# Optimization experiments

Measured on AMD Instinct MI355X. Metric: run time of the kernel, lower is better.

Reference implementation:

```python
import jax, jax.numpy as jnp
import numpy as np

B, S, D, H = 4, 2048, 1024, 16
HD = D // H  # head dim = 64
NEG = jnp.finfo(jnp.float32).min


def setup_inputs() -> dict:
    key = jax.random.key(0)
    ks = jax.random.split(key, 6)
    states = jax.random.normal(ks[0], (B, S, D), dtype=jnp.float32)
    # causal float mask, broadcastable over batch and heads
    mask = jnp.tril(jnp.ones((S, S), dtype=jnp.float32))[None, None, :, :]
    scale = 1.0 / np.sqrt(D)
    Wq = jax.random.normal(ks[1], (D, D), dtype=jnp.float32) * scale
    Wk = jax.random.normal(ks[2], (D, D), dtype=jnp.float32) * scale
    Wv = jax.random.normal(ks[3], (D, D), dtype=jnp.float32) * scale
    Wo = jax.random.normal(ks[4], (D, D), dtype=jnp.float32) * scale
    return {"states": states, "mask": mask, "Wq": Wq, "Wk": Wk, "Wv": Wv, "Wo": Wo}


def _split_heads(x):
    # [B,S,D] -> [B,H,S,HD]
    return x.reshape(B, S, H, HD).transpose(0, 2, 1, 3)


def reference(states, mask, Wq, Wk, Wv, Wo):
    q = _split_heads(states @ Wq)
    k = _split_heads(states @ Wk)
    v = _split_heads(states @ Wv)
    # scores [B,H,S,S], scaled by rsqrt(head_dim) as in the original
    alpha = jnp.einsum("bhqd,bhkd->bhqk", q, k) * (1.0 / jnp.sqrt(jnp.float32(HD)))
    alpha = alpha * mask + (1.0 - mask) * NEG
    alpha = jax.nn.softmax(alpha, axis=-1)
    ctx = jnp.einsum("bhqk,bhkd->bhqd", alpha, v)
    ctx = ctx.transpose(0, 2, 1, 3).reshape(B, S, D)  # concat heads
    return ctx @ Wo
```

## Files before the change

### kernel.cpp

```cpp
#include <hip/hip_runtime.h>
#include <hip/hip_bf16.h>

#define BB 4
#define SS 2048
#define DD 1024
#define HH 16
#define HDD 64
#define MM (BB*SS)

typedef __attribute__((ext_vector_type(8))) short short8;
typedef __attribute__((ext_vector_type(4))) float f32x4;
typedef __attribute__((ext_vector_type(4))) int int4v;
typedef __attribute__((ext_vector_type(4))) short bf16x4;

__device__ __forceinline__ ushort f2bf(float f) {
  union { float f; uint u; } v; v.f = f;
  uint u = v.u;
  uint r = (u + 0x7FFFu + ((u >> 16) & 1u)) >> 16;
  return (ushort)r;
}

__device__ __forceinline__ float exp2f_fast(float x) {
#if __has_builtin(__builtin_amdgcn_exp2f)
  return __builtin_amdgcn_exp2f(x);
#else
  float r; asm("v_exp_f32 %0, %1" : "=v"(r) : "v"(x)); return r;
#endif
}

__device__ __forceinline__ float max3f(float a, float b, float c) {
  return fmaxf(fmaxf(a, b), c);
}

__device__ __forceinline__ bf16x4 pack4bf(float a, float b, float c, float d) {
  union { __hip_bfloat162 h2[2]; bf16x4 s; } u;
  u.h2[0] = __float22bfloat162_rn(make_float2(a, b));
  u.h2[1] = __float22bfloat162_rn(make_float2(c, d));
  return u.s;
}

__device__ __forceinline__ f32x4 mfma16(bf16x4 a, bf16x4 b, f32x4 c) {
#if __has_builtin(__builtin_amdgcn_mfma_f32_16x16x16bf16_1k)
  return __builtin_amdgcn_mfma_f32_16x16x16bf16_1k(a, b, c, 0, 0, 0);
#else
  f32x4 d;
  asm volatile("s_nop 1\n\tv_mfma_f32_16x16x16_bf16 %0, %1, %2, %3\n\ts_nop 7\n\ts_nop 3"
               : "=v"(d) : "v"(a), "v"(b), "v"(c));
  return d;
#endif
}

__device__ __forceinline__ void gload16(void* lds, const void* g) {
  __builtin_amdgcn_global_load_lds((const __attribute__((address_space(1))) void*)g,
                                   (__attribute__((address_space(3))) void*)lds, 16, 0, 0);
}

__global__ __launch_bounds__(256) void k_convert(const float* __restrict__ in,
                                                 ushort* __restrict__ out, int n4) {
  int i = blockIdx.x * 256 + threadIdx.x;
  if (i >= n4) return;
  float4 v = ((const float4*)in)[i];
  uint lo = (uint)f2bf(v.x) | ((uint)f2bf(v.y) << 16);
  uint hi = (uint)f2bf(v.z) | ((uint)f2bf(v.w) << 16);
  ((uint2*)out)[i] = make_uint2(lo, hi);
}

__global__ __launch_bounds__(256) void k_transpose(const float* __restrict__ W0, const float* __restrict__ W1,
                                                   const float* __restrict__ W2, const float* __restrict__ W3,
                                                   ushort* __restrict__ T0, ushort* __restrict__ T1,
                                                   ushort* __restrict__ T2, ushort* __restrict__ T3) {
  __shared__ float t[32][33];
  const float* W; ushort* T;
  switch (blockIdx.z) {
    case 0: W = W0; T = T0; break;
    case 1: W = W1; T = T1; break;
    case 2: W = W2; T = T2; break;
    default: W = W3; T = T3; break;
  }
  float scale = (blockIdx.z == 0) ? 0.18033688011112042f : 1.0f;
  int tx = threadIdx.x, ty = threadIdx.y;
  int x = blockIdx.x * 32 + tx;
  int y0 = blockIdx.y * 32;
#pragma unroll
  for (int j = 0; j < 32; j += 8) t[ty + j][tx] = W[(y0 + ty + j) * DD + x];
  __syncthreads();
#pragma unroll
  for (int j = 0; j < 32; j += 8)
    T[(blockIdx.x * 32 + ty + j) * DD + y0 + tx] = f2bf(t[tx][ty + j] * scale);
}

__global__ __launch_bounds__(256, 2) void k_qkv(const ushort* __restrict__ X,
                                                const ushort* __restrict__ Wqt,
                                                const ushort* __restrict__ Wkt,
                                                const ushort* __restrict__ Wvt,
                                                ushort* __restrict__ Q,
                                                ushort* __restrict__ K,
                                                ushort* __restrict__ Vt) {
  __shared__ ushort Al[2 * 4096];
  __shared__ ushort Bl[3][2 * 4096];
  int tid = threadIdx.x, lane = tid & 63, w = tid >> 6;
  int wm = w >> 1, wn = w & 1, lrow = lane & 15, lgrp = lane >> 4;
  int srow = lane >> 2, scolb = (lane & 3) * 16;
  const char* A8 = (const char*)(X + (size_t)blockIdx.x * 128 * DD);
  const char* B8[3] = { (const char*)(Wqt + (size_t)blockIdx.y * 128 * DD),
                        (const char*)(Wkt + (size_t)blockIdx.y * 128 * DD),
                        (const char*)(Wvt + (size_t)blockIdx.y * 128 * DD) };

  f32x4 acc[3][4][4];
#pragma unroll
  for (int wi = 0; wi < 3; wi++)
#pragma unroll
    for (int i = 0; i < 4; i++)
#pragma unroll
      for (int j = 0; j < 4; j++)
#pragma unroll
        for (int r = 0; r < 4; r++) acc[wi][i][j][r] = 0.f;

#pragma unroll
  for (int ii = 0; ii < 2; ii++) {
    int i = w * 2 + ii;
    size_t ro = (size_t)(i * 16 + srow) * (DD * 2) + scolb;
    gload16(Al + i * 512, A8 + ro);
#pragma unroll
    for (int wi = 0; wi < 3; wi++)
      gload16(&Bl[wi][i * 512], B8[wi] + ro);
  }
  __syncthreads();

  for (int kk = 0; kk < DD; kk += 32) {
    int cur = (kk >> 5) & 1;
    if (kk + 32 < DD) {
#pragma unroll
      for (int ii = 0; ii < 2; ii++) {
        int i = w * 2 + ii;
        size_t ro = (size_t)(i * 16 + srow) * (DD * 2) + (kk + 32) * 2 + scolb;
        gload16(Al + (cur ^ 1) * 4096 + i * 512, A8 + ro);
#pragma unroll
        for (int wi = 0; wi < 3; wi++)
          gload16(&Bl[wi][(cur ^ 1) * 4096 + i * 512], B8[wi] + ro);
      }
    }
    short8 a[4];
#pragma unroll
    for (int i = 0; i < 4; i++)
      a[i] = *(const short8*)&Al[cur * 4096 + (wm * 64 + i * 16 + lrow) * 32 + lgrp * 8];
#pragma unroll
    for (int wi = 0; wi < 3; wi++) {
      short8 b[4];
#pragma unroll
      for (int j = 0; j < 4; j++)
        b[j] = *(const short8*)&Bl[wi][cur * 4096 + (wn * 64 + j * 16 + lrow) * 32 + lgrp * 8];
#pragma unroll
      for (int i = 0; i < 4; i++)
#pragma unroll
        for (int j = 0; j < 4; j++)
          acc[wi][i][j] = __builtin_amdgcn_mfma_f32_16x16x32_bf16(a[i], b[j], acc[wi][i][j], 0, 0, 0);
    }
    __syncthreads();
  }

  int m0 = blockIdx.x * 128 + wm * 64, n0 = blockIdx.y * 128 + wn * 64;
#pragma unroll
  for (int wi = 0; wi < 2; wi++) {
    ushort* Out = (wi == 0) ? Q : K;
#pragma unroll
    for (int i = 0; i < 4; i++)
#pragma unroll
      for (int j = 0; j < 4; j++)
#pragma unroll
        for (int r = 0; r < 4; r++) {
          int row = m0 + i * 16 + lgrp * 4 + r;
          int col = n0 + j * 16 + lrow;
          int b = row >> 11, s = row & 2047, h = col >> 6, hd = col & 63;
          Out[(((size_t)(b * HH + h) * SS) + s) * HDD + hd] = f2bf(acc[wi][i][j][r]);
        }
  }
#pragma unroll
  for (int i = 0; i < 4; i++)
#pragma unroll
    for (int j = 0; j < 4; j++) {
      int row0 = m0 + i * 16 + lgrp * 4;
      int col = n0 + j * 16 + lrow;
      int b = row0 >> 11, s0 = row0 & 2047, h = col >> 6, hd = col & 63;
      bf16x4 s = pack4bf(acc[2][i][j][0], acc[2][i][j][1], acc[2][i][j][2], acc[2][i][j][3]);
      *(bf16x4*)(Vt + (((size_t)(b * HH + h) * HDD) + hd) * SS + s0) = s;
    }
}

#define QB2 64
#define KVB 64
#define NQT2 (SS / QB2)

__global__ __launch_bounds__(128) void k_attn(const ushort* __restrict__ Q,
                                              const ushort* __restrict__ K,
                                              const ushort* __restrict__ Vt,
                                              ushort* __restrict__ Ctx) {
  __shared__ ushort Kl[2][4096];
  __shared__ ushort Vl[2][4096];
  int bid = blockIdx.x;
  int xcd = bid & 7, slot = bid >> 3;
  int j = slot & 15;
  int bh = (slot >> 4) * 8 + xcd;
  int b = bh >> 4, h = bh & 15;
  int tid = threadIdx.x, lane = tid & 63, w = tid >> 6;
  int lrow = lane & 15, lgrp = lane >> 4;

  int srow = lane >> 3;
  int scolb = ((lane & 7) * 16) ^ (srow << 4);
  const char* K8 = (const char*)(K + (size_t)bh * SS * HDD);
  const char* V8 = (const char*)(Vt + (size_t)bh * HDD * SS);

  int kswz = (lrow & 7) << 3;
  int colE[2];
  colE[0] = (lgrp * 8) ^ kswz;
  colE[1] = (lgrp * 8 + 32) ^ kswz;

  const ushort* kc0 = &Kl[0][lrow * 64 + colE[0]];
  const ushort* kc1 = &Kl[0][lrow * 64 + colE[1]];
  const ushort* vbp[4];
#pragma unroll
  for (int t = 0; t < 4; t++) vbp[t] = &Vl[0][lrow * 64 + (((16 * t + lgrp * 4) ^ kswz))];

#pragma unroll
  for (int ph = 0; ph < 2; ph++) {
    int qx = ph == 0 ? (NQT2 - 1 - j) : j;
    int qb = qx * QB2;
    int qw0 = qb + w * 32;
    int ntk = qx + 1;

    const char* kgp[4];
    const char* vgp[4];
#pragma unroll
    for (int ii = 0; ii < 4; ii++) {
      kgp[ii] = K8 + (size_t)(w * 32 + ii * 8 + srow) * 128 + scolb;
      vgp[ii] = V8 + (size_t)(w * 32 + ii * 8 + srow) * (SS * 2) + scolb;
    }

    short8 qf[2][2];
#pragma unroll
    for (int qt = 0; qt < 2; qt++)
#pragma unroll
      for (int c = 0; c < 2; c++)
        qf[qt][c] = *(const short8*)(Q + ((size_t)bh * SS + qb + w * 32 + qt * 16 + lrow) * HDD + lgrp * 8 + 32 * c);

    f32x4 o[2][4];
#pragma unroll
    for (int qt = 0; qt < 2; qt++)
#pragma unroll
      for (int nt = 0; nt < 4; nt++)
#pragma unroll
        for (int r = 0; r < 4; r++) o[qt][nt][r] = 0.f;
    float m_run[2] = {-1e30f, -1e30f}, l_run[2] = {0.f, 0.f};

#pragma unroll
    for (int ii = 0; ii < 4; ii++) {
      gload16(&Kl[0][(w * 4 + ii) * 512], kgp[ii]);
      gload16(&Vl[0][(w * 4 + ii) * 512], vgp[ii]);
      kgp[ii] += KVB * 128;
      vgp[ii] += KVB * 2;
    }
    __syncthreads();

    for (int kt = 0; kt < ntk; kt++) {
      int cur = kt & 1;
      if (kt + 1 < ntk) {
#pragma unroll
        for (int ii = 0; ii < 4; ii++) {
          gload16(&Kl[cur ^ 1][(w * 4 + ii) * 512], kgp[ii]);
          gload16(&Vl[cur ^ 1][(w * 4 + ii) * 512], vgp[ii]);
          kgp[ii] += KVB * 128;
          vgp[ii] += KVB * 2;
        }
      }
      int kb = kt * KVB;
      const ushort* kcc0 = kc0 + (cur << 12);
      const ushort* kcc1 = kc1 + (cur << 12);
      short8 kf[4][2];
#pragma unroll
      for (int t = 0; t < 4; t++) {
        kf[t][0] = *(const short8*)(kcc0 + t * 1024);
        kf[t][1] = *(const short8*)(kcc1 + t * 1024);
      }

      bf16x4 pk[2][4];
#pragma unroll
      for (int qt = 0; qt < 2; qt++) {
        f32x4 st[4];
#pragma unroll
        for (int t = 0; t < 4; t++) {
          f32x4 z;
#pragma unroll
          for (int r = 0; r < 4; r++) z[r] = 0.f;
          z = __builtin_amdgcn_mfma_f32_16x16x32_bf16(kf[t][0], qf[qt][0], z, 0, 0, 0);
          z = __builtin_amdgcn_mfma_f32_16x16x32_bf16(kf[t][1], qf[qt][1], z, 0, 0, 0);
          st[t] = z;
        }
        if (kb + 63 > qw0) {
          int lim = qw0 + qt * 16 + lrow - kb - lgrp * 4;
#pragma unroll
          for (int t = 0; t < 4; t++)
#pragma unroll
            for (int r = 0; r < 4; r++)
              if (16 * t + r > lim) st[t][r] = -1e30f;
        }
        float rm = max3f(st[0][0], st[0][1], st[0][2]);
        rm = max3f(rm, st[0][3], st[1][0]);
        rm = max3f(rm, st[1][1], st[1][2]);
        rm = max3f(rm, st[1][3], st[2][0]);
        rm = max3f(rm, st[2][1], st[2][2]);
        rm = max3f(rm, st[2][3], st[3][0]);
        rm = max3f(rm, st[3][1], st[3][2]);
        rm = fmaxf(rm, st[3][3]);
        rm = fmaxf(rm, __shfl_xor(rm, 16));
        rm = fmaxf(rm, __shfl_xor(rm, 32));
        bool need = rm > m_run[qt] + 8.f;
        if (__any(need)) {
          float mn = need ? rm : m_run[qt];
          float sca = exp2f_fast(m_run[qt] - mn);
          m_run[qt] = mn;
          l_run[qt] *= sca;
#pragma unroll
          for (int nt = 0; nt < 4; nt++)
#pragma unroll
            for (int r = 0; r < 4; r++) o[qt][nt][r] *= sca;
        }
        float m = m_run[qt];
        float rs = 0.f;
#pragma unroll
        for (int t = 0; t < 4; t++) {
          float e0 = exp2f_fast(st[t][0] - m);
          float e1 = exp2f_fast(st[t][1] - m);
          float e2 = exp2f_fast(st[t][2] - m);
          float e3 = exp2f_fast(st[t][3] - m);
          rs += (e0 + e1) + (e2 + e3);
          pk[qt][t] = pack4bf(e0, e1, e2, e3);
        }
        l_run[qt] += rs;
      }

#pragma unroll
      for (int t = 0; t < 4; t++) {
        const ushort* vbt = vbp[t] + (cur << 12);
#pragma unroll
        for (int nt = 0; nt < 4; nt++) {
          bf16x4 va = *(const bf16x4*)(vbt + nt * 1024);
          o[0][nt] = mfma16(va, pk[0][t], o[0][nt]);
          o[1][nt] = mfma16(va, pk[1][t], o[1][nt]);
        }
      }
      __syncthreads();
    }

#pragma unroll
    for (int qt = 0; qt < 2; qt++) {
      float lt = l_run[qt];
      lt += __shfl_xor(lt, 16);
      lt += __shfl_xor(lt, 32);
      float inv = 1.f / lt;
      int q = qb + w * 32 + qt * 16 + lrow;
      ushort* base = Ctx + ((size_t)b * SS + q) * DD + h * HDD;
#pragma unroll
      for (int nt = 0; nt < 4; nt++) {
        bf16x4 s = pack4bf(o[qt][nt][0] * inv, o[qt][nt][1] * inv,
                           o[qt][nt][2] * inv, o[qt][nt][3] * inv);
        *(bf16x4*)(base + nt * 16 + lgrp * 4) = s;
      }
    }
  }
}

__device__ __forceinline__ void gemm_tile(const ushort* __restrict__ Arow,
                                          const ushort* __restrict__ Brow,
                                          ushort* Al, ushort* Bl,
                                          f32x4 acc[4][4]) {
  int tid = threadIdx.x;
  int lane = tid & 63, w = tid >> 6;
  int wm = w >> 1, wn = w & 1;
  int lrow = lane & 15, lgrp = lane >> 4;
#pragma unroll
  for (int i = 0; i < 4; i++)
#pragma unroll
    for (int j = 0; j < 4; j++)
#pragma unroll
      for (int r = 0; r < 4; r++) acc[i][j][r] = 0.f;

  int srow = lane >> 2;
  int scolb = (lane & 3) * 16;
  const char* A8 = (const char*)Arow;
  const char* B8 = (const char*)Brow;

#pragma unroll
  for (int ii = 0; ii < 2; ii++) {
    int i = w * 2 + ii;
    gload16(Al + i * 512, A8 + (size_t)(i * 16 + srow) * (DD * 2) + scolb);
    gload16(Bl + i * 512, B8 + (size_t)(i * 16 + srow) * (DD * 2) + scolb);
  }
  __syncthreads();

  for (int kk = 0; kk < DD; kk += 32) {
    int cur = (kk >> 5) & 1;
    if (kk + 32 < DD) {
#pragma unroll
      for (int ii = 0; ii < 2; ii++) {
        int i = w * 2 + ii;
        gload16(Al + (cur ^ 1) * 4096 + i * 512,
                A8 + (size_t)(i * 16 + srow) * (DD * 2) + (kk + 32) * 2 + scolb);
        gload16(Bl + (cur ^ 1) * 4096 + i * 512,
                B8 + (size_t)(i * 16 + srow) * (DD * 2) + (kk + 32) * 2 + scolb);
      }
    }
    short8 a[4], b[4];
#pragma unroll
    for (int i = 0; i < 4; i++) a[i] = *(const short8*)&Al[cur * 4096 + (wm * 64 + i * 16 + lrow) * 32 + lgrp * 8];
#pragma unroll
    for (int j = 0; j < 4; j++) b[j] = *(const short8*)&Bl[cur * 4096 + (wn * 64 + j * 16 + lrow) * 32 + lgrp * 8];
#pragma unroll
    for (int i = 0; i < 4; i++)
#pragma unroll
      for (int j = 0; j < 4; j++)
        acc[i][j] = __builtin_amdgcn_mfma_f32_16x16x32_bf16(a[i], b[j], acc[i][j], 0, 0, 0);
    __syncthreads();
  }
}

__global__ __launch_bounds__(256) void k_oproj(const ushort* __restrict__ Ctx,
                                               const ushort* __restrict__ Wot,
                                               float* __restrict__ Outp) {
  __shared__ ushort Al[2 * 4096];
  __shared__ ushort Bl[2 * 4096];
  f32x4 acc[4][4];
  gemm_tile(Ctx + (size_t)blockIdx.x * 128 * DD, Wot + (size_t)blockIdx.y * 128 * DD, Al, Bl, acc);
  int lane = threadIdx.x & 63, w = threadIdx.x >> 6;
  int wm = w >> 1, wn = w & 1, lrow = lane & 15, lgrp = lane >> 4;
  int m0 = blockIdx.x * 128 + wm * 64, n0 = blockIdx.y * 128 + wn * 64;
#pragma unroll
  for (int i = 0; i < 4; i++)
#pragma unroll
    for (int j = 0; j < 4; j++)
#pragma unroll
      for (int r = 0; r < 4; r++) {
        int row = m0 + i * 16 + lgrp * 4 + r;
        int col = n0 + j * 16 + lrow;
        Outp[(size_t)row * DD + col] = acc[i][j][r];
      }
}

extern "C" void kernel_launch(void* const* d_in, const int* in_sizes, int n_in,
                              void* d_out, int out_size, void* d_ws, size_t ws_size,
                              hipStream_t stream) {
  const float* states = (const float*)d_in[0];
  const float* Wq = (const float*)d_in[2];
  const float* Wk = (const float*)d_in[3];
  const float* Wv = (const float*)d_in[4];
  const float* Wo = (const float*)d_in[5];
  float* outp = (float*)d_out;

  char* ws = (char*)d_ws;
  const size_t XBF = 0;
  const size_t WQT = 16777216;
  const size_t WKT = WQT + 2097152;
  const size_t WVT = WKT + 2097152;
  const size_t WOT = WVT + 2097152;
  const size_t QO  = WOT + 2097152;
  const size_t KO  = QO + 16777216;
  const size_t VT  = KO + 16777216;
  const size_t CTX = VT + 16777216;

  ushort* Xbf = (ushort*)(ws + XBF);
  ushort* Wqt = (ushort*)(ws + WQT);
  ushort* Wkt = (ushort*)(ws + WKT);
  ushort* Wvt = (ushort*)(ws + WVT);
  ushort* Wot = (ushort*)(ws + WOT);
  ushort* Qb  = (ushort*)(ws + QO);
  ushort* Kb  = (ushort*)(ws + KO);
  ushort* Vtb = (ushort*)(ws + VT);
  ushort* Ctb = (ushort*)(ws + CTX);

  k_convert<<<(MM * DD / 4 + 255) / 256, 256, 0, stream>>>(states, Xbf, MM * DD / 4);
  k_transpose<<<dim3(32, 32, 4), dim3(32, 8), 0, stream>>>(Wq, Wk, Wv, Wo, Wqt, Wkt, Wvt, Wot);
  k_qkv<<<dim3(MM / 128, DD / 128), 256, 0, stream>>>(Xbf, Wqt, Wkt, Wvt, Qb, Kb, Vtb);
  k_attn<<<dim3(NQT2 * BB * HH / 2), 128, 0, stream>>>(Qb, Kb, Vtb, Ctb);
  k_oproj<<<dim3(MM / 128, DD / 128), 256, 0, stream>>>(Ctb, Wot, outp);
}
```

Baseline: 168.3 us.

## Launch one attention block per query tile with single-buffered K/V LDS

Result: slower. 192.3 us (+14.3%).

```diff
diff --git a/kernel.cpp b/kernel.cpp
--- a/kernel.cpp
+++ b/kernel.cpp
@@ -53,6 +53,10 @@
 __device__ __forceinline__ void gload16(void* lds, const void* g) {
   __builtin_amdgcn_global_load_lds((const __attribute__((address_space(1))) void*)g,
                                    (__attribute__((address_space(3))) void*)lds, 16, 0, 0);
+}
+
+__device__ __forceinline__ void drain_vmcnt() {
+  asm volatile("s_waitcnt vmcnt(0)" ::: "memory");
 }
 
 __global__ __launch_bounds__(256) void k_convert(const float* __restrict__ in,
@@ -195,12 +199,12 @@
                                               const ushort* __restrict__ K,
                                               const ushort* __restrict__ Vt,
                                               ushort* __restrict__ Ctx) {
-  __shared__ ushort Kl[2][4096];
-  __shared__ ushort Vl[2][4096];
+  __shared__ ushort Kl[4096];
+  __shared__ ushort Vl[4096];
   int bid = blockIdx.x;
   int xcd = bid & 7, slot = bid >> 3;
-  int j = slot & 15;
-  int bh = (slot >> 4) * 8 + xcd;
+  int qx = NQT2 - 1 - (slot & 31);
+  int bh = (slot >> 5) * 8 + xcd;
   int b = bh >> 4, h = bh & 15;
   int tid = threadIdx.x, lane = tid & 63, w = tid >> 6;
   int lrow = lane & 15, lgrp = lane >> 4;
@@ -215,156 +219,152 @@
   colE[0] = (lgrp * 8) ^ kswz;
   colE[1] = (lgrp * 8 + 32) ^ kswz;
 
-  const ushort* kc0 = &Kl[0][lrow * 64 + colE[0]];
-  const ushort* kc1 = &Kl[0][lrow * 64 + colE[1]];
+  const ushort* kc0 = &Kl[lrow * 64 + colE[0]];
+  const ushort* kc1 = &Kl[lrow * 64 + colE[1]];
   const ushort* vbp[4];
 #pragma unroll
-  for (int t = 0; t < 4; t++) vbp[t] = &Vl[0][lrow * 64 + (((16 * t + lgrp * 4) ^ kswz))];
-
-#pragma unroll
-  for (int ph = 0; ph < 2; ph++) {
-    int qx = ph == 0 ? (NQT2 - 1 - j) : j;
-    int qb = qx * QB2;
-    int qw0 = qb + w * 32;
-    int ntk = qx + 1;
-
-    const char* kgp[4];
-    const char* vgp[4];
-#pragma unroll
-    for (int ii = 0; ii < 4; ii++) {
-      kgp[ii] = K8 + (size_t)(w * 32 + ii * 8 + srow) * 128 + scolb;
-      vgp[ii] = V8 + (size_t)(w * 32 + ii * 8 + srow) * (SS * 2) + scolb;
-    }
-
-    short8 qf[2][2];
-#pragma unroll
-    for (int qt = 0; qt < 2; qt++)
-#pragma unroll
-      for (int c = 0; c < 2; c++)
-        qf[qt][c] = *(const short8*)(Q + ((size_t)bh * SS + qb + w * 32 + qt * 16 + lrow) * HDD + lgrp * 8 + 32 * c);
-
-    f32x4 o[2][4];
-#pragma unroll
-    for (int qt = 0; qt < 2; qt++)
-#pragma unroll
-      for (int nt = 0; nt < 4; nt++)
-#pragma unroll
-        for (int r = 0; r < 4; r++) o[qt][nt][r] = 0.f;
-    float m_run[2] = {-1e30f, -1e30f}, l_run[2] = {0.f, 0.f};
-
-#pragma unroll
-    for (int ii = 0; ii < 4; ii++) {
-      gload16(&Kl[0][(w * 4 + ii) * 512], kgp[ii]);
-      gload16(&Vl[0][(w * 4 + ii) * 512], vgp[ii]);
-      kgp[ii] += KVB * 128;
-      vgp[ii] += KVB * 2;
-    }
+  for (int t = 0; t < 4; t++) vbp[t] = &Vl[lrow * 64 + (((16 * t + lgrp * 4) ^ kswz))];
+
+  int qb = qx * QB2;
+  int qw0 = qb + w * 32;
+  int ntk = qx + 1;
+
+  const char* kgp[4];
+  const char* vgp[4];
+#pragma unroll
+  for (int ii = 0; ii < 4; ii++) {
+    kgp[ii] = K8 + (size_t)(w * 32 + ii * 8 + srow) * 128 + scolb;
+    vgp[ii] = V8 + (size_t)(w * 32 + ii * 8 + srow) * (SS * 2) + scolb;
+  }
+
+  short8 qf[2][2];
+#pragma unroll
+  for (int qt = 0; qt < 2; qt++)
+#pragma unroll
+    for (int c = 0; c < 2; c++)
+      qf[qt][c] = *(const short8*)(Q + ((size_t)bh * SS + qb + w * 32 + qt * 16 + lrow) * HDD + lgrp * 8 + 32 * c);
+
+  f32x4 o[2][4];
+#pragma unroll
+  for (int qt = 0; qt < 2; qt++)
+#pragma unroll
+    for (int nt = 0; nt < 4; nt++)
+#pragma unroll
+      for (int r = 0; r < 4; r++) o[qt][nt][r] = 0.f;
+  float m_run[2] = {-1e30f, -1e30f}, l_run[2] = {0.f, 0.f};
+
+#pragma unroll
+  for (int ii = 0; ii < 4; ii++) {
+    gload16(&Kl[(w * 4 + ii) * 512], kgp[ii]);
+    gload16(&Vl[(w * 4 + ii) * 512], vgp[ii]);
+    kgp[ii] += KVB * 128;
+    vgp[ii] += KVB * 2;
+  }
+  drain_vmcnt();
+
+  for (int kt = 0; kt < ntk; kt++) {
     __syncthreads();
-
-    for (int kt = 0; kt < ntk; kt++) {
-      int cur = kt & 1;
-      if (kt + 1 < ntk) {
-#pragma unroll
-        for (int ii = 0; ii < 4; ii++) {
-          gload16(&Kl[cur ^ 1][(w * 4 + ii) * 512], kgp[ii]);
-          gload16(&Vl[cur ^ 1][(w * 4 + ii) * 512], vgp[ii]);
-          kgp[ii] += KVB * 128;
-          vgp[ii] += KVB * 2;
-        }
-      }
-      int kb = kt * KVB;
-      const ushort* kcc0 = kc0 + (cur << 12);
-      const ushort* kcc1 = kc1 + (cur << 12);
-      short8 kf[4][2];
+    int kb = kt * KVB;
+    short8 kf[4][2];
+#pragma unroll
+    for (int t = 0; t < 4; t++) {
+      kf[t][0] = *(const short8*)(kc0 + t * 1024);
+      kf[t][1] = *(const short8*)(kc1 + t * 1024);
+    }
+
+    bf16x4 pk[2][4];
+#pragma unroll
+    for (int qt = 0; qt < 2; qt++) {
+      f32x4 st[4];
 #pragma unroll
       for (int t = 0; t < 4; t++) {
-        kf[t][0] = *(const short8*)(kcc0 + t * 1024);
-        kf[t][1] = *(const short8*)(kcc1 + t * 1024);
-      }
-
-      bf16x4 pk[2][4];
-#pragma unroll
-      for (int qt = 0; qt < 2; qt++) {
-        f32x4 st[4];
-#pragma unroll
-        for (int t = 0; t < 4; t++) {
-          f32x4 z;
-#pragma unroll
-          for (int r = 0; r < 4; r++) z[r] = 0.f;
-          z = __builtin_amdgcn_mfma_f32_16x16x32_bf16(kf[t][0], qf[qt][0], z, 0, 0, 0);
-          z = __builtin_amdgcn_mfma_f32_16x16x32_bf16(kf[t][1], qf[qt][1], z, 0, 0, 0);
-          st[t] = z;
-        }
-        if (kb + 63 > qw0) {
-          int lim = qw0 + qt * 16 + lrow - kb - lgrp * 4;
-#pragma unroll
-          for (int t = 0; t < 4; t++)
-#pragma unroll
-            for (int r = 0; r < 4; r++)
-              if (16 * t + r > lim) st[t][r] = -1e30f;
-        }
-        float rm = max3f(st[0][0], st[0][1], st[0][2]);
-        rm = max3f(rm, st[0][3], st[1][0]);
-        rm = max3f(rm, st[1][1], st[1][2]);
-        rm = max3f(rm, st[1][3], st[2][0]);
-        rm = max3f(rm, st[2][1], st[2][2]);
-        rm = max3f(rm, st[2][3], st[3][0]);
-        rm = max3f(rm, st[3][1], st[3][2]);
-        rm = fmaxf(rm, st[3][3]);
-        rm = fmaxf(rm, __shfl_xor(rm, 16));
-        rm = fmaxf(rm, __shfl_xor(rm, 32));
-        bool need = rm > m_run[qt] + 8.f;
-        if (__any(need)) {
-          float mn = need ? rm : m_run[qt];
-          float sca = exp2f_fast(m_run[qt] - mn);
-          m_run[qt] = mn;
-          l_run[qt] *= sca;
-#pragma unroll
-          for (int nt = 0; nt < 4; nt++)
-#pragma unroll
-            for (int r = 0; r < 4; r++) o[qt][nt][r] *= sca;
-        }
-        float m = m_run[qt];
-        float rs = 0.f;
-#pragma unroll
-        for (int t = 0; t < 4; t++) {
-          float e0 = exp2f_fast(st[t][0] - m);
-          float e1 = exp2f_fast(st[t][1] - m);
-          float e2 = exp2f_fast(st[t][2] - m);
-          float e3 = exp2f_fast(st[t][3] - m);
-          rs += (e0 + e1) + (e2 + e3);
-          pk[qt][t] = pack4bf(e0, e1, e2, e3);
-        }
-        l_run[qt] += rs;
-      }
-
+        f32x4 z;
+#pragma unroll
+        for (int r = 0; r < 4; r++) z[r] = 0.f;
+        z = __builtin_amdgcn_mfma_f32_16x16x32_bf16(kf[t][0], qf[qt][0], z, 0, 0, 0);
+        z = __builtin_amdgcn_mfma_f32_16x16x32_bf16(kf[t][1], qf[qt][1], z, 0, 0, 0);
+        st[t] = z;
+      }
+      if (kb + 63 > qw0) {
+        int lim = qw0 + qt * 16 + lrow - kb - lgrp * 4;
+#pragma unroll
+        for (int t = 0; t < 4; t++)
+#pragma unroll
+          for (int r = 0; r < 4; r++)
+            if (16 * t + r > lim) st[t][r] = -1e30f;
+      }
+      float rm = max3f(st[0][0], st[0][1], st[0][2]);
+      rm = max3f(rm, st[0][3], st[1][0]);
+      rm = max3f(rm, st[1][1], st[1][2]);
+      rm = max3f(rm, st[1][3], st[2][0]);
+      rm = max3f(rm, st[2][1], st[2][2]);
+      rm = max3f(rm, st[2][3], st[3][0]);
+      rm = max3f(rm, st[3][1], st[3][2]);
+      rm = fmaxf(rm, st[3][3]);
+      rm = fmaxf(rm, __shfl_xor(rm, 16));
+      rm = fmaxf(rm, __shfl_xor(rm, 32));
+      bool need = rm > m_run[qt] + 8.f;
+      if (__any(need)) {
+        float mn = need ? rm : m_run[qt];
+        float sca = exp2f_fast(m_run[qt] - mn);
+        m_run[qt] = mn;
+        l_run[qt] *= sca;
+#pragma unroll
+        for (int nt = 0; nt < 4; nt++)
+#pragma unroll
+          for (int r = 0; r < 4; r++) o[qt][nt][r] *= sca;
+      }
+      float m = m_run[qt];
+      float rs = 0.f;
 #pragma unroll
       for (int t = 0; t < 4; t++) {
-        const ushort* vbt = vbp[t] + (cur << 12);
-#pragma unroll
-        for (int nt = 0; nt < 4; nt++) {
-          bf16x4 va = *(const bf16x4*)(vbt + nt * 1024);
-          o[0][nt] = mfma16(va, pk[0][t], o[0][nt]);
-          o[1][nt] = mfma16(va, pk[1][t], o[1][nt]);
-        }
-      }
+        float e0 = exp2f_fast(st[t][0] - m);
+        float e1 = exp2f_fast(st[t][1] - m);
+        float e2 = exp2f_fast(st[t][2] - m);
+        float e3 = exp2f_fast(st[t][3] - m);
+        rs += (e0 + e1) + (e2 + e3);
+        pk[qt][t] = pack4bf(e0, e1, e2, e3);
+      }
+      l_run[qt] += rs;
+    }
+
+#pragma unroll
+    for (int t = 0; t < 4; t++) {
+      const ushort* vbt = vbp[t];
+#pragma unroll
+      for (int nt = 0; nt < 4; nt++) {
+        bf16x4 va = *(const bf16x4*)(vbt + nt * 1024);
+        o[0][nt] = mfma16(va, pk[0][t], o[0][nt]);
+        o[1][nt] = mfma16(va, pk[1][t], o[1][nt]);
+      }
+    }
+
+    if (kt + 1 < ntk) {
       __syncthreads();
-    }
-
-#pragma unroll
-    for (int qt = 0; qt < 2; qt++) {
-      float lt = l_run[qt];
-      lt += __shfl_xor(lt, 16);
-      lt += __shfl_xor(lt, 32);
-      float inv = 1.f / lt;
-      int q = qb + w * 32 + qt * 16 + lrow;
-      ushort* base = Ctx + ((size_t)b * SS + q) * DD + h * HDD;
-#pragma unroll
-      for (int nt = 0; nt < 4; nt++) {
-        bf16x4 s = pack4bf(o[qt][nt][0] * inv, o[qt][nt][1] * inv,
-                           o[qt][nt][2] * inv, o[qt][nt][3] * inv);
-        *(bf16x4*)(base + nt * 16 + lgrp * 4) = s;
-      }
+#pragma unroll
+      for (int ii = 0; ii < 4; ii++) {
+        gload16(&Kl[(w * 4 + ii) * 512], kgp[ii]);
+        gload16(&Vl[(w * 4 + ii) * 512], vgp[ii]);
+        kgp[ii] += KVB * 128;
+        vgp[ii] += KVB * 2;
+      }
+      drain_vmcnt();
+    }
+  }
+
+#pragma unroll
+  for (int qt = 0; qt < 2; qt++) {
+    float lt = l_run[qt];
+    lt += __shfl_xor(lt, 16);
+    lt += __shfl_xor(lt, 32);
+    float inv = 1.f / lt;
+    int q = qb + w * 32 + qt * 16 + lrow;
+    ushort* base = Ctx + ((size_t)b * SS + q) * DD + h * HDD;
+#pragma unroll
+    for (int nt = 0; nt < 4; nt++) {
+      bf16x4 s = pack4bf(o[qt][nt][0] * inv, o[qt][nt][1] * inv,
+                         o[qt][nt][2] * inv, o[qt][nt][3] * inv);
+      *(bf16x4*)(base + nt * 16 + lgrp * 4) = s;
     }
   }
 }
@@ -479,6 +479,6 @@
   k_convert<<<(MM * DD / 4 + 255) / 256, 256, 0, stream>>>(states, Xbf, MM * DD / 4);
   k_transpose<<<dim3(32, 32, 4), dim3(32, 8), 0, stream>>>(Wq, Wk, Wv, Wo, Wqt, Wkt, Wvt, Wot);
   k_qkv<<<dim3(MM / 128, DD / 128), 256, 0, stream>>>(Xbf, Wqt, Wkt, Wvt, Qb, Kb, Vtb);
-  k_attn<<<dim3(NQT2 * BB * HH / 2), 128, 0, stream>>>(Qb, Kb, Vtb, Ctb);
+  k_attn<<<dim3(NQT2 * BB * HH), 128, 0, stream>>>(Qb, Kb, Vtb, Ctb);
   k_oproj<<<dim3(MM / 128, DD / 128), 256, 0, stream>>>(Ctb, Wot, outp);
 }
```
